# Kernel tuning notes

Measured on AMD Instinct MI355X. Metric: run time of the kernel, lower is better.

## Reference

```python
import jax, jax.numpy as jnp
import numpy as np

B, S, D = 1, 2048, 128   # batch, seq_len, num_hidden (== head dim)
H, KVH = 32, 8           # num_heads, num_kv_heads
REP = H // KVH           # num_rep = 4
D_K = 128                # softmax scale denominator sqrt(d_k)
ROPE_THETA = 10000.0


def _rope(x):
    # x: (B, h, S, D). Standard rotate-half RoPE over last dim, positions on axis -2.
    inv_freq = 1.0 / (ROPE_THETA ** (jnp.arange(0, D, 2, dtype=jnp.float32) / D))  # (D/2,)
    ang = jnp.arange(S, dtype=jnp.float32)[:, None] * inv_freq                      # (S, D/2)
    cos = jnp.concatenate([jnp.cos(ang), jnp.cos(ang)], axis=-1)                    # (S, D)
    sin = jnp.concatenate([jnp.sin(ang), jnp.sin(ang)], axis=-1)
    x1, x2 = jnp.split(x, 2, axis=-1)
    rot = jnp.concatenate([-x2, x1], axis=-1)
    return x * cos + rot * sin


def setup_inputs() -> dict:
    key = jax.random.key(0)
    ks = jax.random.split(key, 11)
    w = 0.02
    return {
        "query":  jax.random.normal(ks[0], (B, S, D), jnp.float32),
        "keys":   jax.random.normal(ks[1], (B, S, D), jnp.float32),
        "values": jax.random.normal(ks[2], (B, S, D), jnp.float32),
        "Wq": jax.random.normal(ks[3], (D, H * D), jnp.float32) * w,
        "bq": jnp.zeros((H * D,), jnp.float32),
        "Wk": jax.random.normal(ks[4], (D, KVH * D), jnp.float32) * w,
        "bk": jnp.zeros((KVH * D,), jnp.float32),
        "Wv": jax.random.normal(ks[5], (D, KVH * D), jnp.float32) * w,
        "bv": jnp.zeros((KVH * D,), jnp.float32),
        "Wo": jax.random.normal(ks[6], (H * D, D), jnp.float32) * w,
        "bo": jnp.zeros((D,), jnp.float32),
    }


def reference(query, keys, values, Wq, bq, Wk, bk, Wv, bv, Wo, bo):
    # Projections; faithful to torch .view(): plain reshape (B,S,h*D)->(B,h,S,D), no transpose.
    q = (query @ Wq + bq).reshape(B, H, S, D)
    k = (keys @ Wk + bk).reshape(B, KVH, S, D)
    v = (values @ Wv + bv).reshape(B, KVH, S, D)
    k = _rope(k)
    v = _rope(v)  # module applies RoPE to values too
    # torch repeat tiles kv heads: q head i <-> kv head (i % KVH).
    qg = q.reshape(B, REP, KVH, S, D)
    scores = jnp.einsum('brgsd,bgtd->brgst', qg, k) / jnp.sqrt(jnp.float32(D_K))
    attn = jax.nn.softmax(scores, axis=-1)  # mask=False path, no causal mask
    out = jnp.einsum('brgst,bgtd->brgsd', attn, v).reshape(B, H, S, D)
    out = out.transpose(0, 2, 1, 3).reshape(B, S, H * D)
    return out @ Wo + bo
```

## Files before the change

kernel.cpp:

```cpp
#include <hip/hip_runtime.h>
#include <math.h>


#define SCALE 0.08838834764831843f
#define L2_10K_64 0.20762050593045952f

typedef short bf16x8 __attribute__((ext_vector_type(8)));
typedef float f32x4 __attribute__((ext_vector_type(4)));

__device__ __forceinline__ unsigned short f2b(float f) {
  union { float f; unsigned u; } x; x.f = f;
  return (unsigned short)((x.u + 0x7FFFu + ((x.u >> 16) & 1u)) >> 16);
}
__device__ __forceinline__ float b2f(unsigned short b) {
  union { unsigned u; float f; } x; x.u = ((unsigned)b) << 16;
  return x.f;
}
__device__ __forceinline__ void lds_dma16(void* lds, const void* g) {
  __builtin_amdgcn_global_load_lds(
      (const __attribute__((address_space(1))) unsigned int*)g,
      (__attribute__((address_space(3))) unsigned int*)lds, 16, 0, 0);
}

__global__ void prep_weights(const float* __restrict__ Wk, const float* __restrict__ Wv,
                             const float* __restrict__ Wo, const float* __restrict__ Wq,
                             const float* __restrict__ bo,
                             unsigned short* __restrict__ Wkt, unsigned short* __restrict__ Wvt,
                             unsigned short* __restrict__ Wot, unsigned short* __restrict__ Wq2,
                             float* __restrict__ out, int big) {
  int b = blockIdx.x, tid = threadIdx.x;
  if (b < 512) {
    int idx = b * 256 + tid;
    int n = idx >> 7, k = idx & 127;
    Wkt[idx] = f2b(Wk[(size_t)k * 1024 + n]);
  } else if (b < 1024) {
    int idx = (b - 512) * 256 + tid;
    int n = idx >> 7, k = idx & 127;
    Wvt[idx] = f2b(Wv[(size_t)k * 1024 + n]);
  } else if (b < 3072) {
    int idx = (b - 1024) * 256 + tid;
    int n = idx >> 12, k = idx & 4095;
    Wot[idx] = f2b(Wo[(size_t)k * 128 + n]);
  } else if (b < 5120) {
    int idx = (b - 3072) * 256 + tid;
    if (big) {
      int n = idx >> 7, k = idx & 127;
      Wq2[idx] = f2b(Wq[(size_t)k * 4096 + n]);
    } else {
      Wq2[idx] = f2b(Wq[idx]);
    }
  } else {
    int idx = (b - 5120) * 256 + tid;
    out[idx] = bo[idx & 127];
  }
}

__global__ __launch_bounds__(256) void proj_kv(const float* __restrict__ keys,
                                               const float* __restrict__ values,
                                               const unsigned short* __restrict__ Wkt,
                                               const unsigned short* __restrict__ Wvt,
                                               const float* __restrict__ bk,
                                               const float* __restrict__ bv,
                                               unsigned short* __restrict__ kp,
                                               unsigned short* __restrict__ vt) {
  int bx = blockIdx.x, m0 = blockIdx.y * 64;
  int vmode = bx >> 3;
  int n0 = (bx & 7) * 128, tb = bx & 7;
  const float* X = vmode ? values : keys;
  const unsigned short* Wt = vmode ? Wvt : Wkt;
  const float* bias = vmode ? bv : bk;
  int tid = threadIdx.x;
  int w = tid >> 6, l = tid & 63;
  int l16 = l & 15, g4 = l >> 4;
  int arow = m0 + w * 16 + l16;
  const f32x4 fz = {0.f, 0.f, 0.f, 0.f};
  f32x4 acc[8];
#pragma unroll
  for (int nb = 0; nb < 8; ++nb) acc[nb] = fz;
#pragma unroll
  for (int kc = 0; kc < 4; ++kc) {
    int kbase = kc * 32 + g4 * 8;
    const float* xp = X + (size_t)arow * 128 + kbase;
    bf16x8 a;
#pragma unroll
    for (int j = 0; j < 8; ++j) a[j] = (short)f2b(xp[j]);
#pragma unroll
    for (int nb = 0; nb < 8; ++nb) {
      bf16x8 b = *(const bf16x8*)(Wt + (size_t)(n0 + nb * 16 + l16) * 128 + kbase);
      acc[nb] = __builtin_amdgcn_mfma_f32_16x16x32_bf16(a, b, acc[nb], 0, 0, 0);
    }
  }
  int d2 = 0;
#pragma unroll
  for (int nb = 0; nb < 4; ++nb) {
    d2 = nb * 16 + l16;
    float invf = exp2f(-(float)d2 * L2_10K_64);
    float blo = bias[n0 + d2], bhi = bias[n0 + d2 + 64];
#pragma unroll
    for (int r = 0; r < 4; ++r) {
      int mi = m0 + w * 16 + g4 * 4 + r;
      int t = (mi & 255) * 8 + tb;
      float ang = (float)t * invf;
      float sf, cf;
      __sincosf(ang, &sf, &cf);
      float x1 = acc[nb][r] + blo;
      float x2 = acc[nb + 4][r] + bhi;
      unsigned short lo = f2b(x1 * cf - x2 * sf);
      unsigned short hi = f2b(x2 * cf + x1 * sf);
      if (vmode) {
        int g = mi >> 8;
        vt[(size_t)g * 262144 + (size_t)d2 * 2048 + t] = lo;
        vt[(size_t)g * 262144 + (size_t)(d2 + 64) * 2048 + t] = hi;
      } else {
        kp[(size_t)mi * 1024 + n0 + d2] = lo;
        kp[(size_t)mi * 1024 + n0 + d2 + 64] = hi;
      }
    }
  }
}

__global__ __launch_bounds__(256) void proj_q(const float* __restrict__ X,
                                              const unsigned short* __restrict__ Wt,
                                              const float* __restrict__ bias,
                                              unsigned short* __restrict__ C) {
  int n0 = blockIdx.x * 64, m0 = blockIdx.y * 64;
  int tid = threadIdx.x;
  int w = tid >> 6, l = tid & 63;
  int l16 = l & 15, g4 = l >> 4;
  int arow = m0 + w * 16 + l16;
  const f32x4 fz = {0.f, 0.f, 0.f, 0.f};
  f32x4 acc[4];
#pragma unroll
  for (int nb = 0; nb < 4; ++nb) acc[nb] = fz;
#pragma unroll
  for (int kc = 0; kc < 4; ++kc) {
    int kbase = kc * 32 + g4 * 8;
    const float* xp = X + (size_t)arow * 128 + kbase;
    bf16x8 a;
#pragma unroll
    for (int j = 0; j < 8; ++j) a[j] = (short)f2b(xp[j]);
#pragma unroll
    for (int nb = 0; nb < 4; ++nb) {
      bf16x8 b = *(const bf16x8*)(Wt + (size_t)(n0 + nb * 16 + l16) * 128 + kbase);
      acc[nb] = __builtin_amdgcn_mfma_f32_16x16x32_bf16(a, b, acc[nb], 0, 0, 0);
    }
  }
#pragma unroll
  for (int nb = 0; nb < 4; ++nb) {
    int n = n0 + nb * 16 + l16;
    float bvv = bias[n];
#pragma unroll
    for (int r = 0; r < 4; ++r)
      C[(size_t)(m0 + w * 16 + g4 * 4 + r) * 4096 + n] = f2b(acc[nb][r] + bvv);
  }
}

__global__ void ws_marker(float* __restrict__ out) {
  out[blockIdx.x * 256 + threadIdx.x] = 12345.0f;
}

template <int FUSED_Q>
__global__ __launch_bounds__(256, 4) void attn_kernel(
    const float* __restrict__ X, const unsigned short* __restrict__ Wqb,
    const float* __restrict__ bq, const unsigned short* __restrict__ qp,
    const unsigned short* __restrict__ kp, const unsigned short* __restrict__ vt,
    const unsigned short* __restrict__ Wot, float* __restrict__ out) {
  __shared__ __align__(16) char smem[37888];
  int bid = blockIdx.x;
  int h = bid & 31, g = h & 7;
  int qi0 = (bid >> 5) * 64;
  int tid = threadIdx.x;
  int w = tid >> 6, l = tid & 63;
  int l16 = l & 15, g4 = l >> 4;

  const f32x4 fz = {0.f, 0.f, 0.f, 0.f};
  bf16x8 qfrag[4];

  if (FUSED_Q) {
    unsigned short* Uni = (unsigned short*)smem;
    int r0 = h * 64 + (qi0 >> 5);
    int col0 = tid * 16;
#pragma unroll
    for (int j = 0; j < 2; ++j) {
      const float* xrow = X + (size_t)(r0 + j) * 128;
      float acc[16];
#pragma unroll
      for (int cc = 0; cc < 16; ++cc) acc[cc] = bq[col0 + cc];
      for (int k = 0; k < 128; ++k) {
        float xv = xrow[k];
        bf16x8 w0 = *(const bf16x8*)(Wqb + (size_t)k * 4096 + col0);
        bf16x8 w1 = *(const bf16x8*)(Wqb + (size_t)k * 4096 + col0 + 8);
#pragma unroll
        for (int e = 0; e < 8; ++e) {
          acc[e] += xv * b2f((unsigned short)w0[e]);
          acc[8 + e] += xv * b2f((unsigned short)w1[e]);
        }
      }
#pragma unroll
      for (int cc = 0; cc < 16; ++cc) Uni[j * 4096 + col0 + cc] = f2b(acc[cc]);
    }
    __syncthreads();
    int srow = w * 16 + l16;
    int sj = srow >> 5, scol = (srow & 31) * 128;
#pragma unroll
    for (int kc = 0; kc < 4; ++kc)
      qfrag[kc] = *(const bf16x8*)&Uni[sj * 4096 + scol + kc * 32 + g4 * 8];
    __syncthreads();
  } else {
    const unsigned short* qrow = qp + ((size_t)h * 2048 + qi0 + w * 16 + l16) * 128;
#pragma unroll
    for (int kc = 0; kc < 4; ++kc)
      qfrag[kc] = *(const bf16x8*)(qrow + kc * 32 + g4 * 8);
  }

  const char* kg = (const char*)(kp + (size_t)g * 262144);
  const char* vg = (const char*)(vt + (size_t)g * 262144);
  unsigned short* PsW = (unsigned short*)(smem + 32768) + w * 640;

#define STAGE_K(tn, kb)                                                          \
  {                                                                              \
    _Pragma("unroll") for (int i = 0; i < 2; ++i) {                              \
      int off = w * 2048 + i * 1024 + l * 16;                                    \
      int row = off >> 8, ch = (off >> 4) & 15;                                  \
      int rch = ch ^ (row & 7);                                                  \
      lds_dma16(smem + (kb) * 8192 + w * 2048 + i * 1024,                        \
                kg + (size_t)(tn) * 8192 + (size_t)row * 256 + rch * 16);        \
    }                                                                            \
  }
#define STAGE_V(tn, vb)                                                          \
  {                                                                              \
    _Pragma("unroll") for (int i = 0; i < 2; ++i) {                              \
      int off = w * 2048 + i * 1024 + l * 16;                                    \
      int vrow = off >> 6, vcb = off & 63;                                       \
      lds_dma16(smem + 16384 + (vb) * 8192 + w * 2048 + i * 1024,                \
                vg + (size_t)vrow * 4096 + (size_t)(tn) * 64 + vcb);             \
    }                                                                            \
  }

  STAGE_K(0, 0);
  STAGE_V(0, 0);
  __syncthreads();

  f32x4 oacc[8];
#pragma unroll
  for (int db = 0; db < 8; ++db) oacc[db] = fz;
  float lacc[4] = {0.f, 0.f, 0.f, 0.f};

  int c = 0;
  for (int t = 0; t < 64; ++t) {
    if (t < 63) {
      STAGE_K(t + 1, c ^ 1);
      STAGE_V(t + 1, c ^ 1);
    }

    f32x4 sacc[2];
    sacc[0] = fz; sacc[1] = fz;
    __builtin_amdgcn_s_setprio(1);
#pragma unroll
    for (int kc = 0; kc < 4; ++kc) {
#pragma unroll
      for (int jb = 0; jb < 2; ++jb) {
        int krow = jb * 16 + l16;
        int rch = (kc * 4 + g4) ^ (krow & 7);
        bf16x8 bfrag = *(const bf16x8*)(smem + c * 8192 + krow * 256 + rch * 16);
        sacc[jb] = __builtin_amdgcn_mfma_f32_16x16x32_bf16(qfrag[kc], bfrag, sacc[jb], 0, 0, 0);
      }
    }
    __builtin_amdgcn_s_setprio(0);
#pragma unroll
    for (int r = 0; r < 4; ++r) {
      unsigned short u0 = f2b(__expf(sacc[0][r] * SCALE));
      unsigned short u1 = f2b(__expf(sacc[1][r] * SCALE));
      lacc[r] += b2f(u0) + b2f(u1);
      PsW[(g4 * 4 + r) * 40 + l16] = u0;
      PsW[(g4 * 4 + r) * 40 + 16 + l16] = u1;
    }
    bf16x8 pfrag = *(const bf16x8*)(PsW + l16 * 40 + g4 * 8);
    __builtin_amdgcn_s_setprio(1);
#pragma unroll
    for (int db = 0; db < 8; ++db) {
      bf16x8 vfrag = *(const bf16x8*)(smem + 16384 + c * 8192 + (db * 16 + l16) * 64 + g4 * 16);
      oacc[db] = __builtin_amdgcn_mfma_f32_16x16x32_bf16(pfrag, vfrag, oacc[db], 0, 0, 0);
    }
    __builtin_amdgcn_s_setprio(0);
    __syncthreads();
    c ^= 1;
  }

#pragma unroll
  for (int r = 0; r < 4; ++r) {
#pragma unroll
    for (int off = 1; off < 16; off <<= 1)
      lacc[r] += __shfl_xor(lacc[r], off, 64);
  }
  float invl[4];
#pragma unroll
  for (int r = 0; r < 4; ++r) invl[r] = 1.f / lacc[r];

  unsigned short* Otile = (unsigned short*)smem;
#pragma unroll
  for (int db = 0; db < 8; ++db) {
#pragma unroll
    for (int r = 0; r < 4; ++r)
      Otile[(w * 16 + g4 * 4 + r) * 136 + db * 16 + l16] = f2b(oacc[db][r] * invl[r]);
  }
  __syncthreads();
  bf16x8 a2[4];
#pragma unroll
  for (int kc = 0; kc < 4; ++kc)
    a2[kc] = *(const bf16x8*)&Otile[(w * 16 + l16) * 136 + kc * 32 + g4 * 8];
  f32x4 acc2[8];
#pragma unroll
  for (int nb = 0; nb < 8; ++nb) acc2[nb] = fz;
#pragma unroll
  for (int kc = 0; kc < 4; ++kc) {
#pragma unroll
    for (int nb = 0; nb < 8; ++nb) {
      bf16x8 b2v = *(const bf16x8*)(Wot + (size_t)(nb * 16 + l16) * 4096 + h * 128 + kc * 32 + g4 * 8);
      acc2[nb] = __builtin_amdgcn_mfma_f32_16x16x32_bf16(a2[kc], b2v, acc2[nb], 0, 0, 0);
    }
  }
#pragma unroll
  for (int nb = 0; nb < 8; ++nb) {
#pragma unroll
    for (int r = 0; r < 4; ++r)
      atomicAdd(&out[(size_t)(qi0 + w * 16 + g4 * 4 + r) * 128 + nb * 16 + l16], acc2[nb][r]);
  }
#undef STAGE_K
#undef STAGE_V
}

extern "C" void kernel_launch(void* const* d_in, const int* in_sizes, int n_in,
                              void* d_out, int out_size, void* d_ws, size_t ws_size,
                              hipStream_t stream) {
  const float* query  = (const float*)d_in[0];
  const float* keys   = (const float*)d_in[1];
  const float* values = (const float*)d_in[2];
  const float* Wq = (const float*)d_in[3];
  const float* bq = (const float*)d_in[4];
  const float* Wk = (const float*)d_in[5];
  const float* bk = (const float*)d_in[6];
  const float* Wv = (const float*)d_in[7];
  const float* bv = (const float*)d_in[8];
  const float* Wo = (const float*)d_in[9];
  const float* bo = (const float*)d_in[10];
  float* out = (float*)d_out;
  char* ws = (char*)d_ws;
  const size_t MB = 1024 * 1024;
  if (ws_size < 10 * MB + 512 * 1024) {
    ws_marker<<<1024, 256, 0, stream>>>(out);
    return;
  }
  unsigned short* Wq2   = (unsigned short*)(ws);
  unsigned short* Wkt   = (unsigned short*)(ws + 1 * MB);
  unsigned short* Wvt   = (unsigned short*)(ws + 1 * MB + 256 * 1024);
  unsigned short* Wot   = (unsigned short*)(ws + 1 * MB + 512 * 1024);
  unsigned short* kproj = (unsigned short*)(ws + 2 * MB + 512 * 1024);
  unsigned short* vt    = (unsigned short*)(ws + 6 * MB + 512 * 1024);
  unsigned short* qproj = (unsigned short*)(ws + 10 * MB + 512 * 1024);
  int big = ws_size >= 27 * MB;

  prep_weights<<<6144, 256, 0, stream>>>(Wk, Wv, Wo, Wq, bo, Wkt, Wvt, Wot, Wq2, out, big);
  proj_kv<<<dim3(16, 32), 256, 0, stream>>>(keys, values, Wkt, Wvt, bk, bv, kproj, vt);

  if (big) {
    proj_q<<<dim3(64, 32), 256, 0, stream>>>(query, Wq2, bq, qproj);
    attn_kernel<0><<<1024, 256, 0, stream>>>(query, Wq2, bq, qproj, kproj, vt, Wot, out);
  } else {
    attn_kernel<1><<<1024, 256, 0, stream>>>(query, Wq2, bq, nullptr, kproj, vt, Wot, out);
  }
}
```

Baseline: 175.7 us.

## Double query rows per attention block and merge Q/KV projection kernels

Each attention block now processes 128 query rows (two 16-row fragments per wave), so every staged K/V tile feeds twice as many MFMAs. The grid halves to 512 blocks and the launch-bounds occupancy hint drops from 4 to 2. The Q and KV projections are merged into one launch, the Q output is written directly in head-major layout, and K is stored in a per-group layout. This cuts K/V staging traffic and launch overhead, in exchange for more register pressure and fewer resident blocks, which reduces latency hiding.

```diff
diff --git a/kernel.cpp b/kernel.cpp
--- a/kernel.cpp
+++ b/kernel.cpp
@@ -55,25 +55,60 @@
   }
 }
 
-__global__ __launch_bounds__(256) void proj_kv(const float* __restrict__ keys,
-                                               const float* __restrict__ values,
-                                               const unsigned short* __restrict__ Wkt,
-                                               const unsigned short* __restrict__ Wvt,
-                                               const float* __restrict__ bk,
-                                               const float* __restrict__ bv,
-                                               unsigned short* __restrict__ kp,
-                                               unsigned short* __restrict__ vt) {
+__global__ __launch_bounds__(256) void proj_all(
+    const float* __restrict__ keys, const float* __restrict__ values,
+    const float* __restrict__ query,
+    const unsigned short* __restrict__ Wkt, const unsigned short* __restrict__ Wvt,
+    const unsigned short* __restrict__ Wqt,
+    const float* __restrict__ bk, const float* __restrict__ bv, const float* __restrict__ bq,
+    unsigned short* __restrict__ kp, unsigned short* __restrict__ vt,
+    unsigned short* __restrict__ qp) {
   int bx = blockIdx.x, m0 = blockIdx.y * 64;
+  int tid = threadIdx.x;
+  int w = tid >> 6, l = tid & 63;
+  int l16 = l & 15, g4 = l >> 4;
+  int arow = m0 + w * 16 + l16;
+  const f32x4 fz = {0.f, 0.f, 0.f, 0.f};
+
+  if (bx >= 16) {
+    int n0 = (bx - 16) * 64;
+    f32x4 acc[4];
+#pragma unroll
+    for (int nb = 0; nb < 4; ++nb) acc[nb] = fz;
+#pragma unroll
+    for (int kc = 0; kc < 4; ++kc) {
+      int kbase = kc * 32 + g4 * 8;
+      const float* xp = query + (size_t)arow * 128 + kbase;
+      bf16x8 a;
+#pragma unroll
+      for (int j = 0; j < 8; ++j) a[j] = (short)f2b(xp[j]);
+#pragma unroll
+      for (int nb = 0; nb < 4; ++nb) {
+        bf16x8 b = *(const bf16x8*)(Wqt + (size_t)(n0 + nb * 16 + l16) * 128 + kbase);
+        acc[nb] = __builtin_amdgcn_mfma_f32_16x16x32_bf16(a, b, acc[nb], 0, 0, 0);
+      }
+    }
+#pragma unroll
+    for (int nb = 0; nb < 4; ++nb) {
+      int n = n0 + nb * 16 + l16;
+      float bvv = bq[n];
+#pragma unroll
+      for (int r = 0; r < 4; ++r) {
+        int mi = m0 + w * 16 + g4 * 4 + r;
+        int h = mi >> 6;
+        int s = ((mi & 63) << 5) | (n >> 7);
+        int d = n & 127;
+        qp[((size_t)h * 2048 + s) * 128 + d] = f2b(acc[nb][r] + bvv);
+      }
+    }
+    return;
+  }
+
   int vmode = bx >> 3;
   int n0 = (bx & 7) * 128, tb = bx & 7;
   const float* X = vmode ? values : keys;
   const unsigned short* Wt = vmode ? Wvt : Wkt;
   const float* bias = vmode ? bv : bk;
-  int tid = threadIdx.x;
-  int w = tid >> 6, l = tid & 63;
-  int l16 = l & 15, g4 = l >> 4;
-  int arow = m0 + w * 16 + l16;
-  const f32x4 fz = {0.f, 0.f, 0.f, 0.f};
   f32x4 acc[8];
 #pragma unroll
   for (int nb = 0; nb < 8; ++nb) acc[nb] = fz;
@@ -90,10 +125,9 @@
       acc[nb] = __builtin_amdgcn_mfma_f32_16x16x32_bf16(a, b, acc[nb], 0, 0, 0);
     }
   }
-  int d2 = 0;
 #pragma unroll
   for (int nb = 0; nb < 4; ++nb) {
-    d2 = nb * 16 + l16;
+    int d2 = nb * 16 + l16;
     float invf = exp2f(-(float)d2 * L2_10K_64);
     float blo = bias[n0 + d2], bhi = bias[n0 + d2 + 64];
 #pragma unroll
@@ -107,51 +141,15 @@
       float x2 = acc[nb + 4][r] + bhi;
       unsigned short lo = f2b(x1 * cf - x2 * sf);
       unsigned short hi = f2b(x2 * cf + x1 * sf);
+      int g = mi >> 8;
       if (vmode) {
-        int g = mi >> 8;
         vt[(size_t)g * 262144 + (size_t)d2 * 2048 + t] = lo;
         vt[(size_t)g * 262144 + (size_t)(d2 + 64) * 2048 + t] = hi;
       } else {
-        kp[(size_t)mi * 1024 + n0 + d2] = lo;
-        kp[(size_t)mi * 1024 + n0 + d2 + 64] = hi;
-      }
-    }
-  }
-}
-
-__global__ __launch_bounds__(256) void proj_q(const float* __restrict__ X,
-                                              const unsigned short* __restrict__ Wt,
-                                              const float* __restrict__ bias,
-                                              unsigned short* __restrict__ C) {
-  int n0 = blockIdx.x * 64, m0 = blockIdx.y * 64;
-  int tid = threadIdx.x;
-  int w = tid >> 6, l = tid & 63;
-  int l16 = l & 15, g4 = l >> 4;
-  int arow = m0 + w * 16 + l16;
-  const f32x4 fz = {0.f, 0.f, 0.f, 0.f};
-  f32x4 acc[4];
-#pragma unroll
-  for (int nb = 0; nb < 4; ++nb) acc[nb] = fz;
-#pragma unroll
-  for (int kc = 0; kc < 4; ++kc) {
-    int kbase = kc * 32 + g4 * 8;
-    const float* xp = X + (size_t)arow * 128 + kbase;
-    bf16x8 a;
-#pragma unroll
-    for (int j = 0; j < 8; ++j) a[j] = (short)f2b(xp[j]);
-#pragma unroll
-    for (int nb = 0; nb < 4; ++nb) {
-      bf16x8 b = *(const bf16x8*)(Wt + (size_t)(n0 + nb * 16 + l16) * 128 + kbase);
-      acc[nb] = __builtin_amdgcn_mfma_f32_16x16x32_bf16(a, b, acc[nb], 0, 0, 0);
-    }
-  }
-#pragma unroll
-  for (int nb = 0; nb < 4; ++nb) {
-    int n = n0 + nb * 16 + l16;
-    float bvv = bias[n];
-#pragma unroll
-    for (int r = 0; r < 4; ++r)
-      C[(size_t)(m0 + w * 16 + g4 * 4 + r) * 4096 + n] = f2b(acc[nb][r] + bvv);
+        kp[(size_t)g * 262144 + (size_t)t * 128 + d2] = lo;
+        kp[(size_t)g * 262144 + (size_t)t * 128 + d2 + 64] = hi;
+      }
+    }
   }
 }
 
@@ -160,62 +158,76 @@
 }
 
 template <int FUSED_Q>
-__global__ __launch_bounds__(256, 4) void attn_kernel(
+__global__ __launch_bounds__(256, 2) void attn_kernel(
     const float* __restrict__ X, const unsigned short* __restrict__ Wqb,
     const float* __restrict__ bq, const unsigned short* __restrict__ qp,
     const unsigned short* __restrict__ kp, const unsigned short* __restrict__ vt,
     const unsigned short* __restrict__ Wot, float* __restrict__ out) {
-  __shared__ __align__(16) char smem[37888];
+  __shared__ __align__(16) char smem[43008];
   int bid = blockIdx.x;
   int h = bid & 31, g = h & 7;
-  int qi0 = (bid >> 5) * 64;
+  int qi0 = (bid >> 5) * 128;
   int tid = threadIdx.x;
   int w = tid >> 6, l = tid & 63;
   int l16 = l & 15, g4 = l >> 4;
 
   const f32x4 fz = {0.f, 0.f, 0.f, 0.f};
-  bf16x8 qfrag[4];
+  bf16x8 qfrag[2][4];
 
   if (FUSED_Q) {
     unsigned short* Uni = (unsigned short*)smem;
     int r0 = h * 64 + (qi0 >> 5);
     int col0 = tid * 16;
 #pragma unroll
-    for (int j = 0; j < 2; ++j) {
-      const float* xrow = X + (size_t)(r0 + j) * 128;
-      float acc[16];
-#pragma unroll
-      for (int cc = 0; cc < 16; ++cc) acc[cc] = bq[col0 + cc];
+    for (int jp = 0; jp < 2; ++jp) {
+      float acc[2][16];
+#pragma unroll
+      for (int j = 0; j < 2; ++j)
+#pragma unroll
+        for (int cc = 0; cc < 16; ++cc) acc[j][cc] = bq[col0 + cc];
+      const float* xr0 = X + (size_t)(r0 + jp * 2) * 128;
+      const float* xr1 = xr0 + 128;
       for (int k = 0; k < 128; ++k) {
-        float xv = xrow[k];
+        float x0 = xr0[k], x1 = xr1[k];
         bf16x8 w0 = *(const bf16x8*)(Wqb + (size_t)k * 4096 + col0);
         bf16x8 w1 = *(const bf16x8*)(Wqb + (size_t)k * 4096 + col0 + 8);
 #pragma unroll
         for (int e = 0; e < 8; ++e) {
-          acc[e] += xv * b2f((unsigned short)w0[e]);
-          acc[8 + e] += xv * b2f((unsigned short)w1[e]);
+          float f0 = b2f((unsigned short)w0[e]), f1 = b2f((unsigned short)w1[e]);
+          acc[0][e] += x0 * f0; acc[0][8 + e] += x0 * f1;
+          acc[1][e] += x1 * f0; acc[1][8 + e] += x1 * f1;
         }
       }
 #pragma unroll
-      for (int cc = 0; cc < 16; ++cc) Uni[j * 4096 + col0 + cc] = f2b(acc[cc]);
+      for (int j = 0; j < 2; ++j)
+#pragma unroll
+        for (int cc = 0; cc < 16; ++cc)
+          Uni[(jp * 2 + j) * 4096 + col0 + cc] = f2b(acc[j][cc]);
     }
     __syncthreads();
-    int srow = w * 16 + l16;
-    int sj = srow >> 5, scol = (srow & 31) * 128;
-#pragma unroll
-    for (int kc = 0; kc < 4; ++kc)
-      qfrag[kc] = *(const bf16x8*)&Uni[sj * 4096 + scol + kc * 32 + g4 * 8];
+#pragma unroll
+    for (int a = 0; a < 2; ++a) {
+      int srow = w * 32 + a * 16 + l16;
+      int sj = srow >> 5, scol = (srow & 31) * 128;
+#pragma unroll
+      for (int kc = 0; kc < 4; ++kc)
+        qfrag[a][kc] = *(const bf16x8*)&Uni[sj * 4096 + scol + kc * 32 + g4 * 8];
+    }
     __syncthreads();
   } else {
-    const unsigned short* qrow = qp + ((size_t)h * 2048 + qi0 + w * 16 + l16) * 128;
-#pragma unroll
-    for (int kc = 0; kc < 4; ++kc)
-      qfrag[kc] = *(const bf16x8*)(qrow + kc * 32 + g4 * 8);
+#pragma unroll
+    for (int a = 0; a < 2; ++a) {
+      const unsigned short* qrow =
+          qp + ((size_t)h * 2048 + qi0 + w * 32 + a * 16 + l16) * 128;
+#pragma unroll
+      for (int kc = 0; kc < 4; ++kc)
+        qfrag[a][kc] = *(const bf16x8*)(qrow + kc * 32 + g4 * 8);
+    }
   }
 
   const char* kg = (const char*)(kp + (size_t)g * 262144);
   const char* vg = (const char*)(vt + (size_t)g * 262144);
-  unsigned short* PsW = (unsigned short*)(smem + 32768) + w * 640;
+  unsigned short* PsW = (unsigned short*)(smem + 32768) + w * 1280;
 
 #define STAGE_K(tn, kb)                                                          \
   {                                                                              \
@@ -241,10 +253,12 @@
   STAGE_V(0, 0);
   __syncthreads();
 
-  f32x4 oacc[8];
-#pragma unroll
-  for (int db = 0; db < 8; ++db) oacc[db] = fz;
-  float lacc[4] = {0.f, 0.f, 0.f, 0.f};
+  f32x4 oacc[2][8];
+#pragma unroll
+  for (int a = 0; a < 2; ++a)
+#pragma unroll
+    for (int db = 0; db < 8; ++db) oacc[a][db] = fz;
+  float lacc[2][4] = {{0.f, 0.f, 0.f, 0.f}, {0.f, 0.f, 0.f, 0.f}};
 
   int c = 0;
   for (int t = 0; t < 64; ++t) {
@@ -253,8 +267,8 @@
       STAGE_V(t + 1, c ^ 1);
     }
 
-    f32x4 sacc[2];
-    sacc[0] = fz; sacc[1] = fz;
+    f32x4 sacc[2][2];
+    sacc[0][0] = fz; sacc[0][1] = fz; sacc[1][0] = fz; sacc[1][1] = fz;
     __builtin_amdgcn_s_setprio(1);
 #pragma unroll
     for (int kc = 0; kc < 4; ++kc) {
@@ -263,69 +277,85 @@
         int krow = jb * 16 + l16;
         int rch = (kc * 4 + g4) ^ (krow & 7);
         bf16x8 bfrag = *(const bf16x8*)(smem + c * 8192 + krow * 256 + rch * 16);
-        sacc[jb] = __builtin_amdgcn_mfma_f32_16x16x32_bf16(qfrag[kc], bfrag, sacc[jb], 0, 0, 0);
+        sacc[0][jb] = __builtin_amdgcn_mfma_f32_16x16x32_bf16(qfrag[0][kc], bfrag, sacc[0][jb], 0, 0, 0);
+        sacc[1][jb] = __builtin_amdgcn_mfma_f32_16x16x32_bf16(qfrag[1][kc], bfrag, sacc[1][jb], 0, 0, 0);
       }
     }
     __builtin_amdgcn_s_setprio(0);
 #pragma unroll
-    for (int r = 0; r < 4; ++r) {
-      unsigned short u0 = f2b(__expf(sacc[0][r] * SCALE));
-      unsigned short u1 = f2b(__expf(sacc[1][r] * SCALE));
-      lacc[r] += b2f(u0) + b2f(u1);
-      PsW[(g4 * 4 + r) * 40 + l16] = u0;
-      PsW[(g4 * 4 + r) * 40 + 16 + l16] = u1;
-    }
-    bf16x8 pfrag = *(const bf16x8*)(PsW + l16 * 40 + g4 * 8);
+    for (int a = 0; a < 2; ++a) {
+#pragma unroll
+      for (int r = 0; r < 4; ++r) {
+        unsigned short u0 = f2b(__expf(sacc[a][0][r] * SCALE));
+        unsigned short u1 = f2b(__expf(sacc[a][1][r] * SCALE));
+        lacc[a][r] += b2f(u0) + b2f(u1);
+        PsW[(a * 16 + g4 * 4 + r) * 40 + l16] = u0;
+        PsW[(a * 16 + g4 * 4 + r) * 40 + 16 + l16] = u1;
+      }
+    }
+    bf16x8 pfrag0 = *(const bf16x8*)(PsW + (l16)*40 + g4 * 8);
+    bf16x8 pfrag1 = *(const bf16x8*)(PsW + (16 + l16) * 40 + g4 * 8);
     __builtin_amdgcn_s_setprio(1);
 #pragma unroll
     for (int db = 0; db < 8; ++db) {
       bf16x8 vfrag = *(const bf16x8*)(smem + 16384 + c * 8192 + (db * 16 + l16) * 64 + g4 * 16);
-      oacc[db] = __builtin_amdgcn_mfma_f32_16x16x32_bf16(pfrag, vfrag, oacc[db], 0, 0, 0);
+      oacc[0][db] = __builtin_amdgcn_mfma_f32_16x16x32_bf16(pfrag0, vfrag, oacc[0][db], 0, 0, 0);
+      oacc[1][db] = __builtin_amdgcn_mfma_f32_16x16x32_bf16(pfrag1, vfrag, oacc[1][db], 0, 0, 0);
     }
     __builtin_amdgcn_s_setprio(0);
     __syncthreads();
     c ^= 1;
   }
 
-#pragma unroll
-  for (int r = 0; r < 4; ++r) {
-#pragma unroll
-    for (int off = 1; off < 16; off <<= 1)
-      lacc[r] += __shfl_xor(lacc[r], off, 64);
-  }
-  float invl[4];
-#pragma unroll
-  for (int r = 0; r < 4; ++r) invl[r] = 1.f / lacc[r];
+  float invl[2][4];
+#pragma unroll
+  for (int a = 0; a < 2; ++a)
+#pragma unroll
+    for (int r = 0; r < 4; ++r) {
+      float v = lacc[a][r];
+#pragma unroll
+      for (int off = 1; off < 16; off <<= 1) v += __shfl_xor(v, off, 64);
+      invl[a][r] = 1.f / v;
+    }
 
   unsigned short* Otile = (unsigned short*)smem;
 #pragma unroll
-  for (int db = 0; db < 8; ++db) {
-#pragma unroll
-    for (int r = 0; r < 4; ++r)
-      Otile[(w * 16 + g4 * 4 + r) * 136 + db * 16 + l16] = f2b(oacc[db][r] * invl[r]);
-  }
+  for (int a = 0; a < 2; ++a)
+#pragma unroll
+    for (int db = 0; db < 8; ++db)
+#pragma unroll
+      for (int r = 0; r < 4; ++r)
+        Otile[(w * 32 + a * 16 + g4 * 4 + r) * 136 + db * 16 + l16] =
+            f2b(oacc[a][db][r] * invl[a][r]);
   __syncthreads();
-  bf16x8 a2[4];
-#pragma unroll
-  for (int kc = 0; kc < 4; ++kc)
-    a2[kc] = *(const bf16x8*)&Otile[(w * 16 + l16) * 136 + kc * 32 + g4 * 8];
-  f32x4 acc2[8];
-#pragma unroll
-  for (int nb = 0; nb < 8; ++nb) acc2[nb] = fz;
+  bf16x8 a2[2][4];
+#pragma unroll
+  for (int a = 0; a < 2; ++a)
+#pragma unroll
+    for (int kc = 0; kc < 4; ++kc)
+      a2[a][kc] = *(const bf16x8*)&Otile[(w * 32 + a * 16 + l16) * 136 + kc * 32 + g4 * 8];
+  f32x4 acc2[2][8];
+#pragma unroll
+  for (int a = 0; a < 2; ++a)
+#pragma unroll
+    for (int nb = 0; nb < 8; ++nb) acc2[a][nb] = fz;
 #pragma unroll
   for (int kc = 0; kc < 4; ++kc) {
 #pragma unroll
     for (int nb = 0; nb < 8; ++nb) {
       bf16x8 b2v = *(const bf16x8*)(Wot + (size_t)(nb * 16 + l16) * 4096 + h * 128 + kc * 32 + g4 * 8);
-      acc2[nb] = __builtin_amdgcn_mfma_f32_16x16x32_bf16(a2[kc], b2v, acc2[nb], 0, 0, 0);
-    }
-  }
-#pragma unroll
-  for (int nb = 0; nb < 8; ++nb) {
-#pragma unroll
-    for (int r = 0; r < 4; ++r)
-      atomicAdd(&out[(size_t)(qi0 + w * 16 + g4 * 4 + r) * 128 + nb * 16 + l16], acc2[nb][r]);
-  }
+      acc2[0][nb] = __builtin_amdgcn_mfma_f32_16x16x32_bf16(a2[0][kc], b2v, acc2[0][nb], 0, 0, 0);
+      acc2[1][nb] = __builtin_amdgcn_mfma_f32_16x16x32_bf16(a2[1][kc], b2v, acc2[1][nb], 0, 0, 0);
+    }
+  }
+#pragma unroll
+  for (int a = 0; a < 2; ++a)
+#pragma unroll
+    for (int nb = 0; nb < 8; ++nb)
+#pragma unroll
+      for (int r = 0; r < 4; ++r)
+        atomicAdd(&out[(size_t)(qi0 + w * 32 + a * 16 + g4 * 4 + r) * 128 + nb * 16 + l16],
+                  acc2[a][nb][r]);
 #undef STAGE_K
 #undef STAGE_V
 }
@@ -361,12 +391,14 @@
   int big = ws_size >= 27 * MB;
 
   prep_weights<<<6144, 256, 0, stream>>>(Wk, Wv, Wo, Wq, bo, Wkt, Wvt, Wot, Wq2, out, big);
-  proj_kv<<<dim3(16, 32), 256, 0, stream>>>(keys, values, Wkt, Wvt, bk, bv, kproj, vt);
 
   if (big) {
-    proj_q<<<dim3(64, 32), 256, 0, stream>>>(query, Wq2, bq, qproj);
-    attn_kernel<0><<<1024, 256, 0, stream>>>(query, Wq2, bq, qproj, kproj, vt, Wot, out);
+    proj_all<<<dim3(80, 32), 256, 0, stream>>>(keys, values, query, Wkt, Wvt, Wq2,
+                                               bk, bv, bq, kproj, vt, qproj);
+    attn_kernel<0><<<512, 256, 0, stream>>>(query, Wq2, bq, qproj, kproj, vt, Wot, out);
   } else {
-    attn_kernel<1><<<1024, 256, 0, stream>>>(query, Wq2, bq, nullptr, kproj, vt, Wot, out);
-  }
-}
+    proj_all<<<dim3(16, 32), 256, 0, stream>>>(keys, values, query, Wkt, Wvt, Wq2,
+                                               bk, bv, bq, kproj, vt, qproj);
+    attn_kernel<1><<<512, 256, 0, stream>>>(query, Wq2, bq, nullptr, kproj, vt, Wot, out);
+  }
+}
```

Result: no change. 173.2 us (-1.5%).
